# Kernel optimization log

Measured on AMD Instinct MI355X. Metric: run time of the kernel, lower is better.

Reference implementation:

```python
import jax, jax.numpy as jnp
import numpy as np

N_EMBD = 1024
B, T = 4, 2048

def setup_inputs() -> dict:
    key = jax.random.key(0)
    k1, k2, k3, k4 = jax.random.split(key, 4)
    s = 1.0 / np.sqrt(N_EMBD)
    return {
        "x": jax.random.normal(k1, (B, T, N_EMBD), dtype=jnp.float32),
        "Wq": jax.random.normal(k2, (N_EMBD, N_EMBD), dtype=jnp.float32) * s,
        "Wk": jax.random.normal(k3, (N_EMBD, N_EMBD), dtype=jnp.float32) * s,
        "Wv": jax.random.normal(k4, (N_EMBD, N_EMBD), dtype=jnp.float32) * s,
    }

def reference(x, Wq, Wk, Wv):
    # x: [B,T,C]; torch Linear (no bias): y = x @ W.T
    Bq, Tq, C = x.shape
    q = jnp.einsum('btc,dc->btd', x, Wq)
    k = jnp.einsum('btc,dc->btd', x, Wk)
    v = jnp.einsum('btc,dc->btd', x, Wv)
    att = jnp.einsum('bqd,bkd->bqk', q, k) / jnp.sqrt(jnp.float32(C))
    causal = jnp.tril(jnp.ones((Tq, Tq), dtype=bool))  # [T,T]
    att = jnp.where(causal, att, -jnp.inf)
    w = jax.nn.softmax(att, axis=-1)
    # dropout is identity in eval mode
    out = jnp.einsum('bqk,bkd->bqd', w, v)
    return out
```

## Files before the change

kernel.cpp:

```cpp
#include <hip/hip_runtime.h>
#include <stdint.h>

typedef __attribute__((ext_vector_type(8))) __bf16 bf16x8;
typedef __attribute__((ext_vector_type(8))) unsigned short ushort8;
typedef __attribute__((ext_vector_type(4))) float f32x4;

static __device__ __forceinline__ unsigned short f2bf(float f) {
  unsigned u = __float_as_uint(f);
  u += 0x7fffu + ((u >> 16) & 1u);
  return (unsigned short)(u >> 16);
}

union U16cast { ushort8 u; bf16x8 b; };
static __device__ __forceinline__ bf16x8 as_bf16x8(ushort8 x) { U16cast t; t.u = x; return t.b; }
static __device__ __forceinline__ bf16x8 ldfrag(const unsigned short* p) {
  return as_bf16x8(*(const ushort8*)p);
}

#define GLD_LDS16(g, l)                                                        \
  __builtin_amdgcn_global_load_lds(                                            \
      (const __attribute__((address_space(1))) void*)(g),                      \
      (__attribute__((address_space(3))) void*)(l), 16, 0, 0)

__global__ __launch_bounds__(256) void cast_all(
    const float* __restrict__ x, const float* __restrict__ Wq,
    const float* __restrict__ Wk, const float* __restrict__ Wv,
    unsigned short* __restrict__ out, float* __restrict__ lzero,
    long nx4, long nw4, long n4) {
  long g = (long)blockIdx.x * blockDim.x + threadIdx.x;
  if (g < 2048) ((float4*)lzero)[g] = (float4){0.f, 0.f, 0.f, 0.f};
  long i = g;
  long stride = (long)gridDim.x * blockDim.x;
  for (; i < n4; i += stride) {
    const float4* src;
    long j = i;
    if (j < nx4) {
      src = (const float4*)x;
    } else {
      j -= nx4;
      if (j < nw4) src = (const float4*)Wq;
      else if (j < 2 * nw4) { src = (const float4*)Wk; j -= nw4; }
      else { src = (const float4*)Wv; j -= 2 * nw4; }
    }
    float4 v = src[j];
    ushort4 o;
    o.x = f2bf(v.x); o.y = f2bf(v.y); o.z = f2bf(v.z); o.w = f2bf(v.w);
    *(ushort4*)(out + i * 4) = o;
  }
}

__global__ __launch_bounds__(512, 4) void gemm_qkv(
    const unsigned short* __restrict__ A, const unsigned short* __restrict__ B,
    unsigned short* __restrict__ qkv, unsigned short* __restrict__ vT) {
  __shared__ __align__(16) unsigned short As[2][4096];
  __shared__ __align__(16) unsigned short Bs[2][8192];

  int wg = blockIdx.x;
  wg = (wg & 7) * 96 + (wg >> 3);
  const int bm = wg / 12, bn = wg % 12;
  const int m0 = bm << 7, n0 = bn << 8;

  const int tid = threadIdx.x;

  const int srow = tid >> 2;
  const int sseg = (tid & 3) ^ ((srow >> 1) & 3);
  const unsigned short* sa = A + (long)(m0 + srow) * 1024 + sseg * 8;
  const unsigned short* sb0 = B + (long)(n0 + srow) * 1024 + sseg * 8;
  const unsigned short* sb1 = sb0 + (long)128 * 1024;
  unsigned short* dA = &As[0][0] + tid * 8;
  unsigned short* dB = &Bs[0][0] + tid * 8;

#define STG(kt, s)                                                             \
  do {                                                                         \
    GLD_LDS16(sa + (kt) * 32, dA + (s) * 4096);                                \
    GLD_LDS16(sb0 + (kt) * 32, dB + (s) * 8192);                               \
    GLD_LDS16(sb1 + (kt) * 32, dB + (s) * 8192 + 4096);                        \
  } while (0)

  const int lane = tid & 63;
  const int w = tid >> 6;
  const int wr = w >> 2;
  const int wc = w & 3;
  const int fr = lane & 15;
  const int kb = lane >> 4;
  const int segr = (kb ^ ((fr >> 1) & 3)) << 3;
  const unsigned short* rA = &As[0][0] + (wr * 64 + fr) * 32 + segr;
  const unsigned short* rB = &Bs[0][0] + (wc * 64 + fr) * 32 + segr;

  f32x4 acc[4][4];
#pragma unroll
  for (int mf = 0; mf < 4; ++mf)
#pragma unroll
    for (int nf = 0; nf < 4; ++nf)
      acc[mf][nf] = (f32x4){0.f, 0.f, 0.f, 0.f};

  STG(0, 0);
  __syncthreads();

  for (int kt = 0; kt < 32; ++kt) {
    const int s = kt & 1;
    if (kt + 1 < 32) STG(kt + 1, s ^ 1);

    const unsigned short* pA = rA + s * 4096;
    const unsigned short* pB = rB + s * 8192;
    bf16x8 av[4], bv[4];
#pragma unroll
    for (int mf = 0; mf < 4; ++mf) av[mf] = ldfrag(pA + mf * 512);
#pragma unroll
    for (int nf = 0; nf < 4; ++nf) bv[nf] = ldfrag(pB + nf * 512);

#pragma unroll
    for (int mf = 0; mf < 4; ++mf)
#pragma unroll
      for (int nf = 0; nf < 4; ++nf)
        acc[mf][nf] = __builtin_amdgcn_mfma_f32_16x16x32_bf16(av[mf], bv[nf], acc[mf][nf], 0, 0, 0);

    __syncthreads();
  }
#undef STG

  const int rq = kb << 2;
  if (n0 < 2048) {
#pragma unroll
    for (int mf = 0; mf < 4; ++mf) {
      const int row = m0 + wr * 64 + mf * 16 + rq;
#pragma unroll
      for (int nf = 0; nf < 4; ++nf) {
        const int col = n0 + wc * 64 + nf * 16 + fr;
#pragma unroll
        for (int r = 0; r < 4; ++r)
          qkv[(long)(row + r) * 3072 + col] = f2bf(acc[mf][nf][r]);
      }
    }
  } else {
    const int b2 = m0 >> 11;
    const int t0 = (m0 & 2047) + wr * 64;
#pragma unroll
    for (int mf = 0; mf < 4; ++mf) {
      const int trow = t0 + mf * 16 + rq;
#pragma unroll
      for (int nf = 0; nf < 4; ++nf) {
        const int colv = (n0 - 2048) + wc * 64 + nf * 16 + fr;
        ushort4 o;
        o.x = f2bf(acc[mf][nf][0]); o.y = f2bf(acc[mf][nf][1]);
        o.z = f2bf(acc[mf][nf][2]); o.w = f2bf(acc[mf][nf][3]);
        *(ushort4*)(vT + ((long)b2 * 1024 + colv) * 2048 + trow) = o;
      }
    }
  }
}

template <int MODE>
__global__ __launch_bounds__(256, 4) void gemm128(
    const unsigned short* __restrict__ A, const unsigned short* __restrict__ Bp,
    void* __restrict__ Cout, float* __restrict__ lbuf) {
  __shared__ __align__(16) unsigned short As[2][4096];
  __shared__ __align__(16) unsigned short Bs[2][4096];

  constexpr int LDA = (MODE == 1) ? 3072 : 2048;

  const int wgid = blockIdx.x;
  int m0, n0, b;
  if constexpr (MODE == 1) {
    b = wgid & 3;
    const int t = wgid >> 2;
    int bm = 0;
    while ((bm + 2) * (bm + 1) / 2 <= t) ++bm;
    const int bn = t - bm * (bm + 1) / 2;
    m0 = bm << 7; n0 = bn << 7;
  } else {
    const int xcd = wgid & 7;
    const int inner = wgid >> 3;
    const int s = inner >> 5;
    const int rem = inner & 31;
    b = rem >> 3;
    const int bn = rem & 7;
    const int bm = s ? (15 - xcd) : xcd;
    m0 = bm << 7; n0 = bn << 7;
  }

  const unsigned short* Ab = A;
  const unsigned short* Bb = Bp;
  if constexpr (MODE == 1) {
    Ab += (long)b * 2048 * 3072;
    Bb += (long)b * 2048 * 3072;
  } else {
    Ab += (long)b * 2048 * 2048;
    Bb += (long)b * 1024 * 2048;
  }

  const int tid = threadIdx.x;

  const int srow = tid >> 2;
  const int sseg = (tid & 3) ^ ((srow >> 1) & 3);
  const unsigned short* sa = Ab + (long)(m0 + srow) * LDA + sseg * 8;
  const unsigned short* sb = Bb + (long)(n0 + srow) * LDA + sseg * 8;
  const long sRj = (long)64 * LDA;
  unsigned short* dA = &As[0][0] + tid * 8;
  unsigned short* dB = &Bs[0][0] + tid * 8;

#define STG(kt, s)                                                             \
  do {                                                                         \
    GLD_LDS16(sa + (kt) * 32, dA + (s) * 4096);                                \
    GLD_LDS16(sa + sRj + (kt) * 32, dA + (s) * 4096 + 2048);                   \
    GLD_LDS16(sb + (kt) * 32, dB + (s) * 4096);                                \
    GLD_LDS16(sb + sRj + (kt) * 32, dB + (s) * 4096 + 2048);                   \
  } while (0)

  const int lane = tid & 63;
  const int w = tid >> 6;
  const int wr = w >> 1;
  const int wc = w & 1;
  const int fr = lane & 15;
  const int kb = lane >> 4;
  const unsigned short* rA0 = &As[0][0] + wr * 64 * 32;
  const unsigned short* rB0 = &Bs[0][0] + wc * 64 * 32;

  f32x4 acc[4][4];
#pragma unroll
  for (int mf = 0; mf < 4; ++mf)
#pragma unroll
    for (int nf = 0; nf < 4; ++nf)
      acc[mf][nf] = (f32x4){0.f, 0.f, 0.f, 0.f};

  const int kend = (MODE == 2) ? (m0 + 128) : 1024;
  const int NT = kend >> 5;

  STG(0, 0);
  __syncthreads();

  for (int kt = 0; kt < NT; ++kt) {
    const int s = kt & 1;
    if (kt + 1 < NT) STG(kt + 1, s ^ 1);

    bf16x8 av[4], bv[4];
#pragma unroll
    for (int mf = 0; mf < 4; ++mf) {
      const int row = mf * 16 + fr;
      const int segr = (kb ^ ((row >> 1) & 3)) << 3;
      av[mf] = ldfrag(rA0 + s * 4096 + row * 32 + segr);
    }
#pragma unroll
    for (int nf = 0; nf < 4; ++nf) {
      const int row = nf * 16 + fr;
      const int segr = (kb ^ ((row >> 1) & 3)) << 3;
      bv[nf] = ldfrag(rB0 + s * 4096 + row * 32 + segr);
    }

#pragma unroll
    for (int mf = 0; mf < 4; ++mf)
#pragma unroll
      for (int nf = 0; nf < 4; ++nf)
        acc[mf][nf] = __builtin_amdgcn_mfma_f32_16x16x32_bf16(av[mf], bv[nf], acc[mf][nf], 0, 0, 0);

    __syncthreads();
  }
#undef STG

  const int rq = kb << 2;
  if constexpr (MODE == 1) {
    unsigned short* Pu = (unsigned short*)Cout + (long)b * 2048 * 2048;
    float* lrow = lbuf + b * 2048;
#pragma unroll
    for (int mf = 0; mf < 4; ++mf) {
      const int row = m0 + wr * 64 + mf * 16 + rq;
      float psum0 = 0.f, psum1 = 0.f, psum2 = 0.f, psum3 = 0.f;
#pragma unroll
      for (int nf = 0; nf < 4; ++nf) {
        const int col = n0 + wc * 64 + nf * 16 + fr;
        float e0 = (col > row + 0) ? 0.f : __expf(acc[mf][nf][0] * 0.03125f);
        float e1 = (col > row + 1) ? 0.f : __expf(acc[mf][nf][1] * 0.03125f);
        float e2 = (col > row + 2) ? 0.f : __expf(acc[mf][nf][2] * 0.03125f);
        float e3 = (col > row + 3) ? 0.f : __expf(acc[mf][nf][3] * 0.03125f);
        psum0 += e0; psum1 += e1; psum2 += e2; psum3 += e3;
        Pu[(long)(row + 0) * 2048 + col] = f2bf(e0);
        Pu[(long)(row + 1) * 2048 + col] = f2bf(e1);
        Pu[(long)(row + 2) * 2048 + col] = f2bf(e2);
        Pu[(long)(row + 3) * 2048 + col] = f2bf(e3);
      }
#pragma unroll
      for (int off = 1; off < 16; off <<= 1) {
        psum0 += __shfl_xor(psum0, off);
        psum1 += __shfl_xor(psum1, off);
        psum2 += __shfl_xor(psum2, off);
        psum3 += __shfl_xor(psum3, off);
      }
      if (fr == 0) {
        atomicAdd(&lrow[row + 0], psum0);
        atomicAdd(&lrow[row + 1], psum1);
        atomicAdd(&lrow[row + 2], psum2);
        atomicAdd(&lrow[row + 3], psum3);
      }
    }
  } else {
    float* Cf = (float*)Cout + (long)b * 2048 * 1024;
    const float* lrow = lbuf + b * 2048;
#pragma unroll
    for (int mf = 0; mf < 4; ++mf) {
      const int row = m0 + wr * 64 + mf * 16 + rq;
      float il0 = 1.0f / lrow[row + 0];
      float il1 = 1.0f / lrow[row + 1];
      float il2 = 1.0f / lrow[row + 2];
      float il3 = 1.0f / lrow[row + 3];
#pragma unroll
      for (int nf = 0; nf < 4; ++nf) {
        const int col = n0 + wc * 64 + nf * 16 + fr;
        Cf[(long)(row + 0) * 1024 + col] = acc[mf][nf][0] * il0;
        Cf[(long)(row + 1) * 1024 + col] = acc[mf][nf][1] * il1;
        Cf[(long)(row + 2) * 1024 + col] = acc[mf][nf][2] * il2;
        Cf[(long)(row + 3) * 1024 + col] = acc[mf][nf][3] * il3;
      }
    }
  }
}

extern "C" void kernel_launch(void* const* d_in, const int* in_sizes, int n_in,
                              void* d_out, int out_size, void* d_ws, size_t ws_size,
                              hipStream_t stream) {
  const float* x  = (const float*)d_in[0];
  const float* Wq = (const float*)d_in[1];
  const float* Wk = (const float*)d_in[2];
  const float* Wv = (const float*)d_in[3];
  float* out = (float*)d_out;

  const int Bb = 4, T = 2048, C = 1024;
  const long BT = (long)Bb * T;
  const int N3 = 3 * C;

  char* ws = (char*)d_ws;
  unsigned short* xb   = (unsigned short*)ws; ws += BT * C * 2;
  unsigned short* wbuf = (unsigned short*)ws; ws += (long)N3 * C * 2;
  unsigned short* qkv  = (unsigned short*)ws; ws += BT * N3 * 2;
  unsigned short* vT   = (unsigned short*)ws; ws += BT * C * 2;
  unsigned short* Pu   = (unsigned short*)ws; ws += (long)Bb * T * T * 2;
  float* lbuf          = (float*)ws;          ws += BT * 4;

  const long nx4 = BT * C / 4, nw4 = (long)C * C / 4;
  cast_all<<<2048, 256, 0, stream>>>(x, Wq, Wk, Wv, xb, lbuf, nx4, nw4, nx4 + 3 * nw4);

  gemm_qkv<<<dim3(768, 1, 1), 512, 0, stream>>>(xb, wbuf, qkv, vT);

  gemm128<1><<<dim3(544, 1, 1), 256, 0, stream>>>(qkv, qkv + C, Pu, lbuf);

  gemm128<2><<<dim3(512, 1, 1), 256, 0, stream>>>(Pu, vT, out, lbuf);
}
```

Baseline: 155.8 us.

## Triple-buffer LDS staging with vmcnt waits and one barrier per k-step

Both GEMM kernels move from double- to triple-buffered LDS tiles loaded with global_load_lds, prefetching two k-steps ahead. Each iteration waits on a partial vmcnt and uses a single raw barrier instead of two __syncthreads, so global loads can overlap more compute. MFMA sections also get raised wave priority through s_setprio. The extra buffer raises LDS use per block (gemm_qkv to about 72KB), which may cut occupancy, and correctness depends on the hand-written vmcnt counts matching the loads each STG issues.

```diff
diff --git a/kernel.cpp b/kernel.cpp
--- a/kernel.cpp
+++ b/kernel.cpp
@@ -52,8 +52,8 @@
 __global__ __launch_bounds__(512, 4) void gemm_qkv(
     const unsigned short* __restrict__ A, const unsigned short* __restrict__ B,
     unsigned short* __restrict__ qkv, unsigned short* __restrict__ vT) {
-  __shared__ __align__(16) unsigned short As[2][4096];
-  __shared__ __align__(16) unsigned short Bs[2][8192];
+  __shared__ __align__(16) unsigned short As[3][4096];
+  __shared__ __align__(16) unsigned short Bs[3][8192];
 
   int wg = blockIdx.x;
   wg = (wg & 7) * 96 + (wg >> 3);
@@ -95,27 +95,35 @@
       acc[mf][nf] = (f32x4){0.f, 0.f, 0.f, 0.f};
 
   STG(0, 0);
-  __syncthreads();
-
+  STG(1, 1);
+
+  int cur = 0, pre = 2;
   for (int kt = 0; kt < 32; ++kt) {
-    const int s = kt & 1;
-    if (kt + 1 < 32) STG(kt + 1, s ^ 1);
-
-    const unsigned short* pA = rA + s * 4096;
-    const unsigned short* pB = rB + s * 8192;
+    if (kt < 31) asm volatile("s_waitcnt vmcnt(3)" ::: "memory");
+    else         asm volatile("s_waitcnt vmcnt(0)" ::: "memory");
+    __builtin_amdgcn_s_barrier();
+    asm volatile("" ::: "memory");
+
+    if (kt < 30) STG(kt + 2, pre);
+
+    const unsigned short* pA = rA + cur * 4096;
+    const unsigned short* pB = rB + cur * 8192;
     bf16x8 av[4], bv[4];
 #pragma unroll
     for (int mf = 0; mf < 4; ++mf) av[mf] = ldfrag(pA + mf * 512);
 #pragma unroll
     for (int nf = 0; nf < 4; ++nf) bv[nf] = ldfrag(pB + nf * 512);
 
+    __builtin_amdgcn_s_setprio(1);
 #pragma unroll
     for (int mf = 0; mf < 4; ++mf)
 #pragma unroll
       for (int nf = 0; nf < 4; ++nf)
         acc[mf][nf] = __builtin_amdgcn_mfma_f32_16x16x32_bf16(av[mf], bv[nf], acc[mf][nf], 0, 0, 0);
-
-    __syncthreads();
+    __builtin_amdgcn_s_setprio(0);
+
+    cur = (cur == 2) ? 0 : cur + 1;
+    pre = (pre == 2) ? 0 : pre + 1;
   }
 #undef STG
 
@@ -154,8 +162,8 @@
 __global__ __launch_bounds__(256, 4) void gemm128(
     const unsigned short* __restrict__ A, const unsigned short* __restrict__ Bp,
     void* __restrict__ Cout, float* __restrict__ lbuf) {
-  __shared__ __align__(16) unsigned short As[2][4096];
-  __shared__ __align__(16) unsigned short Bs[2][4096];
+  __shared__ __align__(16) unsigned short As[3][4096];
+  __shared__ __align__(16) unsigned short Bs[3][4096];
 
   constexpr int LDA = (MODE == 1) ? 3072 : 2048;
 
@@ -227,33 +235,41 @@
   const int NT = kend >> 5;
 
   STG(0, 0);
-  __syncthreads();
-
+  STG(1, 1);
+
+  int cur = 0, pre = 2;
   for (int kt = 0; kt < NT; ++kt) {
-    const int s = kt & 1;
-    if (kt + 1 < NT) STG(kt + 1, s ^ 1);
+    if (kt < NT - 1) asm volatile("s_waitcnt vmcnt(4)" ::: "memory");
+    else             asm volatile("s_waitcnt vmcnt(0)" ::: "memory");
+    __builtin_amdgcn_s_barrier();
+    asm volatile("" ::: "memory");
+
+    if (kt < NT - 2) STG(kt + 2, pre);
 
     bf16x8 av[4], bv[4];
 #pragma unroll
     for (int mf = 0; mf < 4; ++mf) {
       const int row = mf * 16 + fr;
       const int segr = (kb ^ ((row >> 1) & 3)) << 3;
-      av[mf] = ldfrag(rA0 + s * 4096 + row * 32 + segr);
+      av[mf] = ldfrag(rA0 + cur * 4096 + row * 32 + segr);
     }
 #pragma unroll
     for (int nf = 0; nf < 4; ++nf) {
       const int row = nf * 16 + fr;
       const int segr = (kb ^ ((row >> 1) & 3)) << 3;
-      bv[nf] = ldfrag(rB0 + s * 4096 + row * 32 + segr);
-    }
-
+      bv[nf] = ldfrag(rB0 + cur * 4096 + row * 32 + segr);
+    }
+
+    __builtin_amdgcn_s_setprio(1);
 #pragma unroll
     for (int mf = 0; mf < 4; ++mf)
 #pragma unroll
       for (int nf = 0; nf < 4; ++nf)
         acc[mf][nf] = __builtin_amdgcn_mfma_f32_16x16x32_bf16(av[mf], bv[nf], acc[mf][nf], 0, 0, 0);
-
-    __syncthreads();
+    __builtin_amdgcn_s_setprio(0);
+
+    cur = (cur == 2) ? 0 : cur + 1;
+    pre = (pre == 2) ? 0 : pre + 1;
   }
 #undef STG
 
```

Result: slower. 163.3 us (+4.8%).

## Enlarge QKV GEMM tile to 256x256 with interleaved load/MFMA schedule

Applied to the files above, without the earlier changes.

The QKV projection GEMM now uses 256x256 output tiles with a K-step of 64, launching half as many workgroups. Its main loop is software-pipelined: eight phases per two K-steps interleave LDS fragment reads, async global-to-LDS loads and MFMA quarter-blocks, using explicit barriers, vmcnt waits and s_setprio. The aim is more data reuse per LDS byte and better overlap of global loads with matrix math. In exchange it needs 128 KB of LDS and 128 accumulator registers per thread, which cuts occupancy, and the hand-tuned wait counts are fragile.

```diff
diff --git a/kernel.cpp b/kernel.cpp
--- a/kernel.cpp
+++ b/kernel.cpp
@@ -49,33 +49,75 @@
   }
 }
 
-__global__ __launch_bounds__(512, 4) void gemm_qkv(
+
+template <int BUF, int MH>
+static __device__ __forceinline__ void ds_a(const unsigned short* lA0,
+                                            const unsigned short* lA1,
+                                            bf16x8 (&av)[4][2]) {
+#pragma unroll
+  for (int mf = 0; mf < 4; ++mf) {
+    av[mf][0] = ldfrag(lA0 + BUF * 16384 + MH * 4096 + mf * 1024);
+    av[mf][1] = ldfrag(lA1 + BUF * 16384 + MH * 4096 + mf * 1024);
+  }
+}
+
+template <int BUF, int NH>
+static __device__ __forceinline__ void ds_b(const unsigned short* lB0,
+                                            const unsigned short* lB1,
+                                            bf16x8 (&bvn)[2][2]) {
+#pragma unroll
+  for (int nf = 0; nf < 2; ++nf) {
+    bvn[nf][0] = ldfrag(lB0 + BUF * 16384 + NH * 2048 + nf * 1024);
+    bvn[nf][1] = ldfrag(lB1 + BUF * 16384 + NH * 2048 + nf * 1024);
+  }
+}
+
+template <int MH, int NH>
+static __device__ __forceinline__ void mfma16(const bf16x8 (&av)[4][2],
+                                              const bf16x8 (&bvn)[2][2],
+                                              f32x4 (&acc)[8][4]) {
+#pragma unroll
+  for (int k = 0; k < 2; ++k)
+#pragma unroll
+    for (int mf = 0; mf < 4; ++mf)
+#pragma unroll
+      for (int nf = 0; nf < 2; ++nf)
+        acc[MH * 4 + mf][NH * 2 + nf] = __builtin_amdgcn_mfma_f32_16x16x32_bf16(
+            av[mf][k], bvn[nf][k], acc[MH * 4 + mf][NH * 2 + nf], 0, 0, 0);
+}
+
+static __device__ __forceinline__ void bar_pre() {
+  __builtin_amdgcn_s_barrier();
+  asm volatile("s_waitcnt lgkmcnt(0)" ::: "memory");
+  __builtin_amdgcn_sched_barrier(0);
+  __builtin_amdgcn_s_setprio(1);
+}
+static __device__ __forceinline__ void bar_post() {
+  __builtin_amdgcn_s_setprio(0);
+  __builtin_amdgcn_s_barrier();
+}
+
+__global__ __launch_bounds__(512, 2) void gemm_qkv(
     const unsigned short* __restrict__ A, const unsigned short* __restrict__ B,
     unsigned short* __restrict__ qkv, unsigned short* __restrict__ vT) {
-  __shared__ __align__(16) unsigned short As[2][4096];
-  __shared__ __align__(16) unsigned short Bs[2][8192];
+  __shared__ __align__(16) unsigned short As[2][16384];
+  __shared__ __align__(16) unsigned short Bs[2][16384];
 
   int wg = blockIdx.x;
-  wg = (wg & 7) * 96 + (wg >> 3);
+  wg = (wg & 7) * 48 + (wg >> 3);
   const int bm = wg / 12, bn = wg % 12;
-  const int m0 = bm << 7, n0 = bn << 8;
+  const int m0 = bm << 8, n0 = bn << 8;
 
   const int tid = threadIdx.x;
-
-  const int srow = tid >> 2;
-  const int sseg = (tid & 3) ^ ((srow >> 1) & 3);
-  const unsigned short* sa = A + (long)(m0 + srow) * 1024 + sseg * 8;
-  const unsigned short* sb0 = B + (long)(n0 + srow) * 1024 + sseg * 8;
-  const unsigned short* sb1 = sb0 + (long)128 * 1024;
-  unsigned short* dA = &As[0][0] + tid * 8;
-  unsigned short* dB = &Bs[0][0] + tid * 8;
-
-#define STG(kt, s)                                                             \
-  do {                                                                         \
-    GLD_LDS16(sa + (kt) * 32, dA + (s) * 4096);                                \
-    GLD_LDS16(sb0 + (kt) * 32, dB + (s) * 8192);                               \
-    GLD_LDS16(sb1 + (kt) * 32, dB + (s) * 8192 + 4096);                        \
-  } while (0)
+  const int t8 = tid * 8;
+
+  const int srow = tid >> 3;
+  const int gseg = (tid & 7) ^ (srow & 7);
+  const unsigned short* pA = A + (long)(m0 + srow) * 1024 + gseg * 8;
+  const unsigned short* pB = B + (long)(n0 + srow) * 1024 + gseg * 8;
+
+#define STG_A(j, tb, kt) GLD_LDS16(pA + (j) * 65536 + (kt) * 64, &As[tb][0] + (j) * 4096 + t8)
+#define STG_B(j, tb, kt) GLD_LDS16(pB + (j) * 65536 + (kt) * 64, &Bs[tb][0] + (j) * 4096 + t8)
 
   const int lane = tid & 63;
   const int w = tid >> 6;
@@ -83,67 +125,104 @@
   const int wc = w & 3;
   const int fr = lane & 15;
   const int kb = lane >> 4;
-  const int segr = (kb ^ ((fr >> 1) & 3)) << 3;
-  const unsigned short* rA = &As[0][0] + (wr * 64 + fr) * 32 + segr;
-  const unsigned short* rB = &Bs[0][0] + (wc * 64 + fr) * 32 + segr;
-
-  f32x4 acc[4][4];
-#pragma unroll
-  for (int mf = 0; mf < 4; ++mf)
+  const int s0 = kb ^ (fr & 7);
+  const unsigned short* lA0 = &As[0][0] + (wr * 128 + fr) * 64 + (s0 << 3);
+  const unsigned short* lA1 = &As[0][0] + (wr * 128 + fr) * 64 + ((s0 ^ 4) << 3);
+  const unsigned short* lB0 = &Bs[0][0] + (wc * 64 + fr) * 64 + (s0 << 3);
+  const unsigned short* lB1 = &Bs[0][0] + (wc * 64 + fr) * 64 + ((s0 ^ 4) << 3);
+
+  f32x4 acc[8][4];
+#pragma unroll
+  for (int mf = 0; mf < 8; ++mf)
 #pragma unroll
     for (int nf = 0; nf < 4; ++nf)
       acc[mf][nf] = (f32x4){0.f, 0.f, 0.f, 0.f};
 
-  STG(0, 0);
-  __syncthreads();
-
-  for (int kt = 0; kt < 32; ++kt) {
-    const int s = kt & 1;
-    if (kt + 1 < 32) STG(kt + 1, s ^ 1);
-
-    const unsigned short* pA = rA + s * 4096;
-    const unsigned short* pB = rB + s * 8192;
-    bf16x8 av[4], bv[4];
-#pragma unroll
-    for (int mf = 0; mf < 4; ++mf) av[mf] = ldfrag(pA + mf * 512);
-#pragma unroll
-    for (int nf = 0; nf < 4; ++nf) bv[nf] = ldfrag(pB + nf * 512);
-
-#pragma unroll
-    for (int mf = 0; mf < 4; ++mf)
-#pragma unroll
-      for (int nf = 0; nf < 4; ++nf)
-        acc[mf][nf] = __builtin_amdgcn_mfma_f32_16x16x32_bf16(av[mf], bv[nf], acc[mf][nf], 0, 0, 0);
-
-    __syncthreads();
-  }
-#undef STG
+  bf16x8 av[4][2];
+  bf16x8 bv[2][2][2];
+
+  STG_A(0, 0, 0); STG_A(2, 0, 0);
+  STG_B(0, 0, 0); STG_B(2, 0, 0);
+  STG_B(1, 0, 0); STG_B(3, 0, 0);
+  STG_A(1, 0, 0); STG_A(3, 0, 0);
+  asm volatile("s_waitcnt vmcnt(0)" ::: "memory");
+  __builtin_amdgcn_s_barrier();
+
+#pragma unroll 1
+  for (int i = 0; i < 8; ++i) {
+    const int kt1 = 2 * i + 1, kt2 = 2 * i + 2;
+    const bool nl = (i != 7);
+
+    ds_a<0, 0>(lA0, lA1, av);
+    ds_b<0, 0>(lB0, lB1, bv[0]);
+    STG_A(0, 1, kt1); STG_A(2, 1, kt1);
+    bar_pre(); mfma16<0, 0>(av, bv[0], acc); bar_post();
+
+    ds_b<0, 1>(lB0, lB1, bv[1]);
+    STG_B(0, 1, kt1); STG_B(2, 1, kt1);
+    asm volatile("s_waitcnt vmcnt(4)" ::: "memory");
+    bar_pre(); mfma16<0, 1>(av, bv[1], acc); bar_post();
+
+    ds_a<0, 1>(lA0, lA1, av);
+    STG_B(1, 1, kt1); STG_B(3, 1, kt1);
+    bar_pre(); mfma16<1, 0>(av, bv[0], acc); bar_post();
+
+    STG_A(1, 1, kt1); STG_A(3, 1, kt1);
+    asm volatile("s_waitcnt vmcnt(2)" ::: "memory");
+    bar_pre(); mfma16<1, 1>(av, bv[1], acc); bar_post();
+
+    ds_a<1, 0>(lA0, lA1, av);
+    ds_b<1, 0>(lB0, lB1, bv[0]);
+    if (nl) { STG_A(0, 0, kt2); STG_A(2, 0, kt2); }
+    bar_pre(); mfma16<0, 0>(av, bv[0], acc); bar_post();
+
+    ds_b<1, 1>(lB0, lB1, bv[1]);
+    if (nl) {
+      STG_B(0, 0, kt2); STG_B(2, 0, kt2);
+      asm volatile("s_waitcnt vmcnt(4)" ::: "memory");
+    } else {
+      asm volatile("s_waitcnt vmcnt(0)" ::: "memory");
+    }
+    bar_pre(); mfma16<0, 1>(av, bv[1], acc); bar_post();
+
+    ds_a<1, 1>(lA0, lA1, av);
+    if (nl) { STG_B(1, 0, kt2); STG_B(3, 0, kt2); }
+    bar_pre(); mfma16<1, 0>(av, bv[0], acc); bar_post();
+
+    if (nl) {
+      STG_A(1, 0, kt2); STG_A(3, 0, kt2);
+      asm volatile("s_waitcnt vmcnt(2)" ::: "memory");
+    }
+    bar_pre(); mfma16<1, 1>(av, bv[1], acc); bar_post();
+  }
+#undef STG_A
+#undef STG_B
 
   const int rq = kb << 2;
   if (n0 < 2048) {
 #pragma unroll
-    for (int mf = 0; mf < 4; ++mf) {
-      const int row = m0 + wr * 64 + mf * 16 + rq;
-#pragma unroll
-      for (int nf = 0; nf < 4; ++nf) {
-        const int col = n0 + wc * 64 + nf * 16 + fr;
+    for (int mfg = 0; mfg < 8; ++mfg) {
+      const int row = m0 + wr * 128 + mfg * 16 + rq;
+#pragma unroll
+      for (int nfg = 0; nfg < 4; ++nfg) {
+        const int col = n0 + wc * 64 + nfg * 16 + fr;
 #pragma unroll
         for (int r = 0; r < 4; ++r)
-          qkv[(long)(row + r) * 3072 + col] = f2bf(acc[mf][nf][r]);
+          qkv[(long)(row + r) * 3072 + col] = f2bf(acc[mfg][nfg][r]);
       }
     }
   } else {
     const int b2 = m0 >> 11;
-    const int t0 = (m0 & 2047) + wr * 64;
-#pragma unroll
-    for (int mf = 0; mf < 4; ++mf) {
-      const int trow = t0 + mf * 16 + rq;
-#pragma unroll
-      for (int nf = 0; nf < 4; ++nf) {
-        const int colv = (n0 - 2048) + wc * 64 + nf * 16 + fr;
+    const int t0 = (m0 & 2047) + wr * 128;
+#pragma unroll
+    for (int mfg = 0; mfg < 8; ++mfg) {
+      const int trow = t0 + mfg * 16 + rq;
+#pragma unroll
+      for (int nfg = 0; nfg < 4; ++nfg) {
+        const int colv = (n0 - 2048) + wc * 64 + nfg * 16 + fr;
         ushort4 o;
-        o.x = f2bf(acc[mf][nf][0]); o.y = f2bf(acc[mf][nf][1]);
-        o.z = f2bf(acc[mf][nf][2]); o.w = f2bf(acc[mf][nf][3]);
+        o.x = f2bf(acc[mfg][nfg][0]); o.y = f2bf(acc[mfg][nfg][1]);
+        o.z = f2bf(acc[mfg][nfg][2]); o.w = f2bf(acc[mfg][nfg][3]);
         *(ushort4*)(vT + ((long)b2 * 1024 + colv) * 2048 + trow) = o;
       }
     }
@@ -233,7 +312,7 @@
     const int s = kt & 1;
     if (kt + 1 < NT) STG(kt + 1, s ^ 1);
 
-    bf16x8 av[4], bv[4];
+    bf16x8 av[4], bvv[4];
 #pragma unroll
     for (int mf = 0; mf < 4; ++mf) {
       const int row = mf * 16 + fr;
@@ -244,14 +323,14 @@
     for (int nf = 0; nf < 4; ++nf) {
       const int row = nf * 16 + fr;
       const int segr = (kb ^ ((row >> 1) & 3)) << 3;
-      bv[nf] = ldfrag(rB0 + s * 4096 + row * 32 + segr);
+      bvv[nf] = ldfrag(rB0 + s * 4096 + row * 32 + segr);
     }
 
 #pragma unroll
     for (int mf = 0; mf < 4; ++mf)
 #pragma unroll
       for (int nf = 0; nf < 4; ++nf)
-        acc[mf][nf] = __builtin_amdgcn_mfma_f32_16x16x32_bf16(av[mf], bv[nf], acc[mf][nf], 0, 0, 0);
+        acc[mf][nf] = __builtin_amdgcn_mfma_f32_16x16x32_bf16(av[mf], bvv[nf], acc[mf][nf], 0, 0, 0);
 
     __syncthreads();
   }
@@ -338,7 +417,7 @@
   const long nx4 = BT * C / 4, nw4 = (long)C * C / 4;
   cast_all<<<2048, 256, 0, stream>>>(x, Wq, Wk, Wv, xb, lbuf, nx4, nw4, nx4 + 3 * nw4);
 
-  gemm_qkv<<<dim3(768, 1, 1), 512, 0, stream>>>(xb, wbuf, qkv, vT);
+  gemm_qkv<<<dim3(384, 1, 1), 512, 0, stream>>>(xb, wbuf, qkv, vT);
 
   gemm128<1><<<dim3(544, 1, 1), 256, 0, stream>>>(qkv, qkv + C, Pu, lbuf);
 
```

After: 161.9 us. 3.9% more time.

## Restructure QKV GEMM to 256x128 tiles with triple-buffered staggered loads

Applied to the files above, without the earlier changes.

The QKV projection GEMM changes from 512-thread 128x256 tiles to 256-thread 256x128 tiles, where each wave computes a 128x64 output with 8x4 accumulators. The LDS staging becomes triple-buffered, with A loaded one step ahead and B two steps ahead, synchronised by explicit vmcnt waits and raw barriers. The MFMA work is split into two halves with s_setprio raised around each to interleave loads and math. The aim is higher per-wave arithmetic intensity and better overlap of global-to-LDS traffic with compute, at the cost of more registers and LDS and lower occupancy.

```diff
diff --git a/kernel.cpp b/kernel.cpp
--- a/kernel.cpp
+++ b/kernel.cpp
@@ -49,81 +49,106 @@
   }
 }
 
-__global__ __launch_bounds__(512, 4) void gemm_qkv(
+__global__ __launch_bounds__(256, 2) void gemm_qkv(
     const unsigned short* __restrict__ A, const unsigned short* __restrict__ B,
     unsigned short* __restrict__ qkv, unsigned short* __restrict__ vT) {
-  __shared__ __align__(16) unsigned short As[2][4096];
-  __shared__ __align__(16) unsigned short Bs[2][8192];
+  __shared__ __align__(16) unsigned short As[3][8192];
+  __shared__ __align__(16) unsigned short Bs[3][4096];
 
   int wg = blockIdx.x;
   wg = (wg & 7) * 96 + (wg >> 3);
-  const int bm = wg / 12, bn = wg % 12;
-  const int m0 = bm << 7, n0 = bn << 8;
+  const int bm = wg / 24, bn = wg % 24;
+  const int m0 = bm << 8, n0 = bn << 7;
 
   const int tid = threadIdx.x;
-
   const int srow = tid >> 2;
-  const int sseg = (tid & 3) ^ ((srow >> 1) & 3);
-  const unsigned short* sa = A + (long)(m0 + srow) * 1024 + sseg * 8;
-  const unsigned short* sb0 = B + (long)(n0 + srow) * 1024 + sseg * 8;
-  const unsigned short* sb1 = sb0 + (long)128 * 1024;
+  const int gseg = (tid & 3) ^ ((srow >> 1) & 3);
+  const unsigned short* pA = A + (long)(m0 + srow) * 1024 + gseg * 8;
+  const unsigned short* pB = B + (long)(n0 + srow) * 1024 + gseg * 8;
   unsigned short* dA = &As[0][0] + tid * 8;
   unsigned short* dB = &Bs[0][0] + tid * 8;
 
-#define STG(kt, s)                                                             \
+#define STG_A(kt, ab)                                                          \
   do {                                                                         \
-    GLD_LDS16(sa + (kt) * 32, dA + (s) * 4096);                                \
-    GLD_LDS16(sb0 + (kt) * 32, dB + (s) * 8192);                               \
-    GLD_LDS16(sb1 + (kt) * 32, dB + (s) * 8192 + 4096);                        \
+    GLD_LDS16(pA + (kt) * 32,          dA + (ab) * 8192);                      \
+    GLD_LDS16(pA + 65536 + (kt) * 32,  dA + (ab) * 8192 + 2048);               \
+    GLD_LDS16(pA + 131072 + (kt) * 32, dA + (ab) * 8192 + 4096);               \
+    GLD_LDS16(pA + 196608 + (kt) * 32, dA + (ab) * 8192 + 6144);               \
+  } while (0)
+#define STG_B(kt, bb)                                                          \
+  do {                                                                         \
+    GLD_LDS16(pB + (kt) * 32,         dB + (bb) * 4096);                       \
+    GLD_LDS16(pB + 65536 + (kt) * 32, dB + (bb) * 4096 + 2048);                \
   } while (0)
 
   const int lane = tid & 63;
   const int w = tid >> 6;
-  const int wr = w >> 2;
-  const int wc = w & 3;
+  const int wr = w >> 1;
+  const int wc = w & 1;
   const int fr = lane & 15;
   const int kb = lane >> 4;
   const int segr = (kb ^ ((fr >> 1) & 3)) << 3;
-  const unsigned short* rA = &As[0][0] + (wr * 64 + fr) * 32 + segr;
+  const unsigned short* rA = &As[0][0] + (wr * 128 + fr) * 32 + segr;
   const unsigned short* rB = &Bs[0][0] + (wc * 64 + fr) * 32 + segr;
 
-  f32x4 acc[4][4];
-#pragma unroll
-  for (int mf = 0; mf < 4; ++mf)
+  f32x4 acc[8][4];
+#pragma unroll
+  for (int mf = 0; mf < 8; ++mf)
 #pragma unroll
     for (int nf = 0; nf < 4; ++nf)
       acc[mf][nf] = (f32x4){0.f, 0.f, 0.f, 0.f};
 
-  STG(0, 0);
-  __syncthreads();
-
+  STG_A(0, 0);
+  STG_B(0, 0);
+  STG_B(1, 1);
+
+  int c0 = 0, c1 = 1, c2 = 2;
+#pragma unroll 1
   for (int kt = 0; kt < 32; ++kt) {
-    const int s = kt & 1;
-    if (kt + 1 < 32) STG(kt + 1, s ^ 1);
-
-    const unsigned short* pA = rA + s * 4096;
-    const unsigned short* pB = rB + s * 8192;
-    bf16x8 av[4], bv[4];
-#pragma unroll
-    for (int mf = 0; mf < 4; ++mf) av[mf] = ldfrag(pA + mf * 512);
-#pragma unroll
-    for (int nf = 0; nf < 4; ++nf) bv[nf] = ldfrag(pB + nf * 512);
-
+    if (kt < 31) STG_A(kt + 1, c1);
+    if (kt < 31) asm volatile("s_waitcnt vmcnt(6)" ::: "memory");
+    else         asm volatile("s_waitcnt vmcnt(0)" ::: "memory");
+    __builtin_amdgcn_s_barrier();
+    asm volatile("" ::: "memory");
+
+    const unsigned short* pa = rA + c0 * 8192;
+    const unsigned short* pb = rB + c0 * 4096;
+    bf16x8 av0[4], av1[4], bv[4];
+#pragma unroll
+    for (int mf = 0; mf < 4; ++mf) av0[mf] = ldfrag(pa + mf * 512);
+#pragma unroll
+    for (int nf = 0; nf < 4; ++nf) bv[nf] = ldfrag(pb + nf * 512);
+
+    __builtin_amdgcn_s_setprio(1);
 #pragma unroll
     for (int mf = 0; mf < 4; ++mf)
 #pragma unroll
       for (int nf = 0; nf < 4; ++nf)
-        acc[mf][nf] = __builtin_amdgcn_mfma_f32_16x16x32_bf16(av[mf], bv[nf], acc[mf][nf], 0, 0, 0);
-
-    __syncthreads();
-  }
-#undef STG
+        acc[mf][nf] = __builtin_amdgcn_mfma_f32_16x16x32_bf16(av0[mf], bv[nf], acc[mf][nf], 0, 0, 0);
+    __builtin_amdgcn_s_setprio(0);
+
+    if (kt < 30) STG_B(kt + 2, c2);
+#pragma unroll
+    for (int mf = 0; mf < 4; ++mf) av1[mf] = ldfrag(pa + 2048 + mf * 512);
+
+    __builtin_amdgcn_s_setprio(1);
+#pragma unroll
+    for (int mf = 0; mf < 4; ++mf)
+#pragma unroll
+      for (int nf = 0; nf < 4; ++nf)
+        acc[4 + mf][nf] = __builtin_amdgcn_mfma_f32_16x16x32_bf16(av1[mf], bv[nf], acc[4 + mf][nf], 0, 0, 0);
+    __builtin_amdgcn_s_setprio(0);
+
+    const int t = c0; c0 = c1; c1 = c2; c2 = t;
+  }
+#undef STG_A
+#undef STG_B
 
   const int rq = kb << 2;
   if (n0 < 2048) {
 #pragma unroll
-    for (int mf = 0; mf < 4; ++mf) {
-      const int row = m0 + wr * 64 + mf * 16 + rq;
+    for (int mf = 0; mf < 8; ++mf) {
+      const int row = m0 + wr * 128 + mf * 16 + rq;
 #pragma unroll
       for (int nf = 0; nf < 4; ++nf) {
         const int col = n0 + wc * 64 + nf * 16 + fr;
@@ -134,9 +159,9 @@
     }
   } else {
     const int b2 = m0 >> 11;
-    const int t0 = (m0 & 2047) + wr * 64;
-#pragma unroll
-    for (int mf = 0; mf < 4; ++mf) {
+    const int t0 = (m0 & 2047) + wr * 128;
+#pragma unroll
+    for (int mf = 0; mf < 8; ++mf) {
       const int trow = t0 + mf * 16 + rq;
 #pragma unroll
       for (int nf = 0; nf < 4; ++nf) {
@@ -233,7 +258,7 @@
     const int s = kt & 1;
     if (kt + 1 < NT) STG(kt + 1, s ^ 1);
 
-    bf16x8 av[4], bv[4];
+    bf16x8 av[4], bvv[4];
 #pragma unroll
     for (int mf = 0; mf < 4; ++mf) {
       const int row = mf * 16 + fr;
@@ -244,14 +269,14 @@
     for (int nf = 0; nf < 4; ++nf) {
       const int row = nf * 16 + fr;
       const int segr = (kb ^ ((row >> 1) & 3)) << 3;
-      bv[nf] = ldfrag(rB0 + s * 4096 + row * 32 + segr);
+      bvv[nf] = ldfrag(rB0 + s * 4096 + row * 32 + segr);
     }
 
 #pragma unroll
     for (int mf = 0; mf < 4; ++mf)
 #pragma unroll
       for (int nf = 0; nf < 4; ++nf)
-        acc[mf][nf] = __builtin_amdgcn_mfma_f32_16x16x32_bf16(av[mf], bv[nf], acc[mf][nf], 0, 0, 0);
+        acc[mf][nf] = __builtin_amdgcn_mfma_f32_16x16x32_bf16(av[mf], bvv[nf], acc[mf][nf], 0, 0, 0);
 
     __syncthreads();
   }
@@ -338,7 +363,7 @@
   const long nx4 = BT * C / 4, nw4 = (long)C * C / 4;
   cast_all<<<2048, 256, 0, stream>>>(x, Wq, Wk, Wv, xb, lbuf, nx4, nw4, nx4 + 3 * nw4);
 
-  gemm_qkv<<<dim3(768, 1, 1), 512, 0, stream>>>(xb, wbuf, qkv, vT);
+  gemm_qkv<<<dim3(768, 1, 1), 256, 0, stream>>>(xb, wbuf, qkv, vT);
 
   gemm128<1><<<dim3(544, 1, 1), 256, 0, stream>>>(qkv, qkv + C, Pu, lbuf);
 
```

Result: slower. 160.1 us (+2.8%).
